# Kernel tuning notes

Measured on AMD Instinct MI355X. Metric: run time of the kernel, lower is better.

Reference implementation:

```python
import jax, jax.numpy as jnp
import numpy as np

NI = 627   # num_inputs (hardcoded 627 in original forward)
NH = 1024  # num_hidden
EPS_BN = 1e-5

def get_mask(in_f, out_f, nf, mask_type=None):
    in_deg = np.arange(in_f) % nf
    out_deg = np.arange(out_f) % nf
    if mask_type == 'output':
        out_deg = out_deg - 1
    return jnp.asarray((out_deg[:, None] >= in_deg[None, :]).astype(np.float32))

M_IN = get_mask(NI, NH, NI, 'input')        # [NH, NI]
M_H = get_mask(NH, NH, NI)                  # [NH, NH]
M_OUT = get_mask(NH, 2 * NI, NI, 'output')  # [2*NI, NH]

def masked_linear(x, W, b, mask):
    return x @ (W * mask).T + b

def conv1x1(x, W, b):
    # x: [B,C,L], W: [O,C] (kernel_size=1 conv == pointwise channel mix)
    return jnp.einsum('bcl,oc->bol', x, W) + b[None, :, None]

def bn_train(x, g, b):
    # BatchNorm1d training-mode: biased batch stats over (N, L)
    m = x.mean(axis=(0, 2), keepdims=True)
    v = x.var(axis=(0, 2), keepdims=True)
    return (x - m) * jax.lax.rsqrt(v + EPS_BN) * g[None, :, None] + b[None, :, None]

def setup_inputs() -> dict:
    key = jax.random.key(0)
    ks = iter(jax.random.split(key, 32))
    B = 512
    inputs = jax.random.randint(next(ks), (B, NI), 0, 300).astype(jnp.float32)
    def lin(k, o, i):
        return jax.random.normal(k, (o, i), jnp.float32) / np.sqrt(i)
    d = {'inputs': inputs}
    d['W_in'] = lin(next(ks), NH, NI); d['b_in'] = jnp.zeros((NH,), jnp.float32)
    d['W_h1'] = lin(next(ks), NH, NH); d['b_h1'] = jnp.zeros((NH,), jnp.float32)
    d['W_h2'] = lin(next(ks), NH, NH); d['b_h2'] = jnp.zeros((NH,), jnp.float32)
    d['W_out'] = lin(next(ks), 2 * NI, NH); d['b_out'] = jnp.zeros((2 * NI,), jnp.float32)
    chans = [(90, 1), (180, 90), (180, 180), (180, 180), (300, 180)]
    for idx, (o, c) in enumerate(chans, 1):
        d[f'cw{idx}'] = lin(next(ks), o, c)
        d[f'cb{idx}'] = jnp.zeros((o,), jnp.float32)
        if idx < 5:
            d[f'g{idx}'] = jnp.ones((o,), jnp.float32)
            d[f'be{idx}'] = jnp.zeros((o,), jnp.float32)
    return d

def reference(inputs, W_in, b_in, W_h1, b_h1, W_h2, b_h2, W_out, b_out,
              cw1, cb1, g1, be1, cw2, cb2, g2, be2, cw3, cb3, g3, be3,
              cw4, cb4, g4, be4, cw5, cb5):
    # MADE joiner + trunk (trunk = [act, ML, act, ML, ML_out])
    h = masked_linear(inputs, W_in, b_in, M_IN)
    h = jax.nn.relu(h)
    h = masked_linear(h, W_h1, b_h1, M_H)
    h = jax.nn.relu(h)
    h = masked_linear(h, W_h2, b_h2, M_H)
    out = masked_linear(h, W_out, b_out, M_OUT)      # [B, 2*NI]
    gamma_raw, theta = jnp.split(out, 2, axis=1)
    gamma = jax.nn.sigmoid(gamma_raw[:, 2:])          # [B, NI-2]
    # 1x1-conv / BN / ReLU trunk over theta viewed as [B,1,NI]
    x = theta[:, None, :]
    x = jax.nn.relu(bn_train(conv1x1(x, cw1, cb1), g1, be1))
    x = jax.nn.relu(bn_train(conv1x1(x, cw2, cb2), g2, be2))
    x = jax.nn.relu(bn_train(conv1x1(x, cw3, cb3), g3, be3))
    x = jax.nn.relu(bn_train(conv1x1(x, cw4, cb4), g4, be4))
    pred = conv1x1(x, cw5, cb5)                       # [B, 300, NI]
    logp = jax.nn.log_softmax(pred, axis=1)
    tgt = inputs.astype(jnp.int32)                    # [B, NI] class ids
    nll = -jnp.take_along_axis(logp, tgt[:, None, :], axis=1)[:, 0, :]  # [B, NI]
    ll = jnp.where(inputs[:, 2:] > 0,
                   0.1 * jnp.log(gamma + 1e-10) - nll[:, 2:],
                   0.1 * jnp.log(1.0 - gamma + 1e-10)).sum(axis=-1, keepdims=True)
    # mean cross-entropy over first two pixels (scalar, default reduction='mean')
    ll = ll - nll[:, :2].mean()
    return ll
```

## Files before the change

kernel.cpp:

```cpp
#include <hip/hip_runtime.h>
#include <hip/hip_bf16.h>
#include <math.h>

#define BATCH 512
#define NI 627
#define NH 1024
#define NOUTF 1254
#define LLEN 627
#define NBL (512 * 627)
#define EPSBN 1e-5f
#define NSLOT 10240
#define NRED2 40
#define NRED34 20

typedef __attribute__((ext_vector_type(8))) short bf16x8;
typedef __attribute__((ext_vector_type(4))) float f32x4;
typedef unsigned int uint32;
typedef unsigned short ushort16;

__device__ inline short f2b(float x) {
  __hip_bfloat16 h = __float2bfloat16(x);
  return *reinterpret_cast<short*>(&h);
}
__device__ inline float b2f(short s) {
  return __uint_as_float(((uint32)(ushort16)s) << 16);
}
__device__ inline f32x4 mfma16(bf16x8 a, bf16x8 b, f32x4 c) {
  return __builtin_amdgcn_mfma_f32_16x16x32_bf16(a, b, c, 0, 0, 0);
}
__device__ inline bf16x8 zero8() {
  bf16x8 z;
#pragma unroll
  for (int i = 0; i < 8; ++i) z[i] = 0;
  return z;
}
__device__ inline bf16x8 buildx1r(float4 alo, float4 ahi, float4 blo, float4 bhi, float th) {
  bf16x8 r;
  r[0] = f2b(fmaxf(fmaf(alo.x, th, blo.x), 0.f));
  r[1] = f2b(fmaxf(fmaf(alo.y, th, blo.y), 0.f));
  r[2] = f2b(fmaxf(fmaf(alo.z, th, blo.z), 0.f));
  r[3] = f2b(fmaxf(fmaf(alo.w, th, blo.w), 0.f));
  r[4] = f2b(fmaxf(fmaf(ahi.x, th, bhi.x), 0.f));
  r[5] = f2b(fmaxf(fmaf(ahi.y, th, bhi.y), 0.f));
  r[6] = f2b(fmaxf(fmaf(ahi.z, th, bhi.z), 0.f));
  r[7] = f2b(fmaxf(fmaf(ahi.w, th, bhi.w), 0.f));
  return r;
}
__device__ inline bf16x8 buildx1(const float* __restrict__ A1v, const float* __restrict__ B1v,
                                 int k0, float th) {
  float4 alo = *reinterpret_cast<const float4*>(&A1v[k0]);
  float4 ahi = *reinterpret_cast<const float4*>(&A1v[k0 + 4]);
  float4 blo = *reinterpret_cast<const float4*>(&B1v[k0]);
  float4 bhi = *reinterpret_cast<const float4*>(&B1v[k0 + 4]);
  return buildx1r(alo, ahi, blo, bhi, th);
}

__device__ inline void prep_mlpw_elem(const float* W, short* Wb, int i,
                                      int Nreal, int Kreal, int Kpad, int mode) {
  int n = i / Kpad, k = i - n * Kpad;
  float w = 0.f;
  if (n < Nreal && k < Kreal) {
    int od = n >= 627 ? n - 627 : n;
    int kd = k >= 627 ? k - 627 : k;
    bool keep = (mode == 0) ? (od >= k) : (mode == 1) ? (od >= kd) : (od > kd);
    if (keep) w = W[n * Kreal + k];
  }
  Wb[i] = f2b(w);
}
__device__ inline void prep_convw_elem(const float* W, short* Wb, int i,
                                       int Oreal, int Kreal, int Kpad) {
  int o = i / Kpad, k = i - o * Kpad;
  Wb[i] = (o < Oreal && k < Kreal) ? f2b(W[o * Kreal + k]) : (short)0;
}

#define PB_INB   1280
#define PB_WB1   (PB_INB + 2560)
#define PB_WB2   (PB_WB1 + 4096)
#define PB_WB3   (PB_WB2 + 4096)
#define PB_WB4   (PB_WB3 + 5120)
#define PB_CW2   (PB_WB4 + 72)
#define PB_CW3   (PB_CW2 + 144)
#define PB_CW4   (PB_CW3 + 144)
#define PB_CW5   (PB_CW4 + 240)
#define PB_CB    (PB_CW5 + 2)

__global__ __launch_bounds__(256) void prep_all(
    const float* __restrict__ inputs, short* __restrict__ INB,
    const float* __restrict__ W_in, short* __restrict__ WB1,
    const float* __restrict__ W_h1, short* __restrict__ WB2,
    const float* __restrict__ W_h2, short* __restrict__ WB3,
    const float* __restrict__ W_out, short* __restrict__ WB4,
    const float* __restrict__ cw2, short* __restrict__ CW2B,
    const float* __restrict__ cw3, short* __restrict__ CW3B,
    const float* __restrict__ cw4, short* __restrict__ CW4B,
    const float* __restrict__ cw5, short* __restrict__ CW5B,
    const float* __restrict__ cb2, const float* __restrict__ cb3,
    const float* __restrict__ cb4, const float* __restrict__ cb5,
    float* __restrict__ cb2p, float* __restrict__ cb3p,
    float* __restrict__ cb4p, float* __restrict__ cb5p)
{
  const int bid = blockIdx.x;
  if (bid < PB_INB) {
    int i = bid * 256 + threadIdx.x;
    if (i < 512 * 640) {
      int m = i / 640, k = i - m * 640;
      INB[i] = (k < NI) ? f2b(inputs[m * NI + k]) : (short)0;
    }
  } else if (bid < PB_WB1) {
    int i = (bid - PB_INB) * 256 + threadIdx.x;
    if (i < 1024 * 640) prep_mlpw_elem(W_in, WB1, i, 1024, 627, 640, 0);
  } else if (bid < PB_WB2) {
    int i = (bid - PB_WB1) * 256 + threadIdx.x;
    prep_mlpw_elem(W_h1, WB2, i, 1024, 1024, 1024, 1);
  } else if (bid < PB_WB3) {
    int i = (bid - PB_WB2) * 256 + threadIdx.x;
    prep_mlpw_elem(W_h2, WB3, i, 1024, 1024, 1024, 1);
  } else if (bid < PB_WB4) {
    int i = (bid - PB_WB3) * 256 + threadIdx.x;
    if (i < 1280 * 1024) prep_mlpw_elem(W_out, WB4, i, 1254, 1024, 1024, 2);
  } else if (bid < PB_CW2) {
    int i = (bid - PB_WB4) * 256 + threadIdx.x;
    if (i < 192 * 96) prep_convw_elem(cw2, CW2B, i, 180, 90, 96);
  } else if (bid < PB_CW3) {
    int i = (bid - PB_CW2) * 256 + threadIdx.x;
    if (i < 192 * 192) prep_convw_elem(cw3, CW3B, i, 180, 180, 192);
  } else if (bid < PB_CW4) {
    int i = (bid - PB_CW3) * 256 + threadIdx.x;
    if (i < 192 * 192) prep_convw_elem(cw4, CW4B, i, 180, 180, 192);
  } else if (bid < PB_CW5) {
    int i = (bid - PB_CW4) * 256 + threadIdx.x;
    if (i < 320 * 192) prep_convw_elem(cw5, CW5B, i, 300, 180, 192);
  } else {
    int c = (bid - PB_CW5) * 256 + threadIdx.x;
    if (c < 192) {
      cb2p[c] = (c < 180) ? cb2[c] : 0.f;
      cb3p[c] = (c < 180) ? cb3[c] : 0.f;
      cb4p[c] = (c < 180) ? cb4[c] : 0.f;
    }
    if (c < 320) cb5p[c] = (c < 300) ? cb5[c] : 0.f;
  }
}

template<int KPAD>
__global__ __launch_bounds__(256) void mlp_mfma(
    const short* __restrict__ A, const short* __restrict__ Wb, const float* __restrict__ bias,
    float* __restrict__ Cf, short* __restrict__ Cb, int Nreal, int relu)
{
  __shared__ float red[2][2][2][4][64];
  const int tid = threadIdx.x;
  const int l = tid & 63, wv = tid >> 6;
  const int wn = wv >> 1, kh = wv & 1;
  const int m0 = blockIdx.y * 32;
  const int n0 = blockIdx.x * 64 + wn * 32;
  const int lr = l & 15, lk = (l >> 4) * 8, lm4 = (l >> 4) * 4;
  f32x4 acc[2][2] = {};
  constexpr int khalf = KPAD >> 1;
  constexpr int nk = khalf >> 5;
#pragma unroll
  for (int ks = 0; ks < nk; ++ks) {
    int k0 = kh * khalf + ks * 32 + lk;
    bf16x8 a0 = *reinterpret_cast<const bf16x8*>(&A[(size_t)(m0 + lr) * KPAD + k0]);
    bf16x8 a1 = *reinterpret_cast<const bf16x8*>(&A[(size_t)(m0 + 16 + lr) * KPAD + k0]);
    bf16x8 b0 = *reinterpret_cast<const bf16x8*>(&Wb[(size_t)(n0 + lr) * KPAD + k0]);
    bf16x8 b1 = *reinterpret_cast<const bf16x8*>(&Wb[(size_t)(n0 + 16 + lr) * KPAD + k0]);
    acc[0][0] = mfma16(a0, b0, acc[0][0]);
    acc[0][1] = mfma16(a0, b1, acc[0][1]);
    acc[1][0] = mfma16(a1, b0, acc[1][0]);
    acc[1][1] = mfma16(a1, b1, acc[1][1]);
  }
  if (kh == 1) {
#pragma unroll
    for (int mi = 0; mi < 2; ++mi)
#pragma unroll
      for (int nj = 0; nj < 2; ++nj)
#pragma unroll
        for (int r = 0; r < 4; ++r) red[wn][mi][nj][r][l] = acc[mi][nj][r];
  }
  __syncthreads();
  if (kh == 0) {
#pragma unroll
    for (int mi = 0; mi < 2; ++mi)
#pragma unroll
      for (int nj = 0; nj < 2; ++nj) {
        int n = n0 + nj * 16 + lr;
        if (n >= Nreal) continue;
        float bi = bias[n];
#pragma unroll
        for (int r = 0; r < 4; ++r) {
          int m = m0 + mi * 16 + lm4 + r;
          float v = acc[mi][nj][r] + red[wn][mi][nj][r][l] + bi;
          if (relu) v = fmaxf(v, 0.f);
          if (Cb) Cb[(size_t)m * Nreal + n] = f2b(v);
          else Cf[(size_t)m * Nreal + n] = v;
        }
      }
  }
}

__global__ __launch_bounds__(256) void theta_stats(const float* __restrict__ outb, float* __restrict__ tstat)
{
  int b = blockIdx.x;
  const float* th = outb + (size_t)b * NOUTF + NI;
  float s = 0.f, q = 0.f;
  for (int l = threadIdx.x; l < LLEN; l += 256) { float t = th[l]; s += t; q += t * t; }
  for (int off = 1; off < 64; off <<= 1) { s += __shfl_xor(s, off); q += __shfl_xor(q, off); }
  __shared__ float tmp[8];
  int w = threadIdx.x >> 6;
  if ((threadIdx.x & 63) == 0) { tmp[w] = s; tmp[4 + w] = q; }
  __syncthreads();
  if (threadIdx.x == 0) {
    atomicAdd(&tstat[0], tmp[0] + tmp[1] + tmp[2] + tmp[3]);
    atomicAdd(&tstat[1], tmp[4] + tmp[5] + tmp[6] + tmp[7]);
  }
}

__global__ void finalize_conv1(const float* __restrict__ tstat, const float* __restrict__ cw1,
                               const float* __restrict__ g1, const float* __restrict__ be1,
                               float* __restrict__ a1, float* __restrict__ b1)
{
  int c = threadIdx.x;
  if (c >= 96) return;
  if (c < 90) {
    float mt = tstat[0] / (float)NBL;
    float vt = tstat[1] / (float)NBL - mt * mt;
    float w = cw1[c];
    float rs = rsqrtf(w * w * vt + EPSBN);
    float a = w * g1[c] * rs;
    a1[c] = a;
    b1[c] = be1[c] - a * mt;
  } else { a1[c] = 0.f; b1[c] = 0.f; }
}

__global__ __launch_bounds__(192) void bn_reduce1(const float* __restrict__ Sp, const float* __restrict__ Qp,
                                                  float* __restrict__ Sred, float* __restrict__ Qred)
{
  int c = threadIdx.x;
  if (c >= 180) return;
  int base = blockIdx.x * 256;
  float s = 0.f, q = 0.f;
  for (int r = 0; r < 256; ++r) {
    s += Sp[(size_t)(base + r) * 180 + c];
    q += Qp[(size_t)(base + r) * 180 + c];
  }
  Sred[blockIdx.x * 180 + c] = s;
  Qred[blockIdx.x * 180 + c] = q;
}

__global__ void finalize_bn2(const float* __restrict__ Sred, const float* __restrict__ Qred,
                             const float* __restrict__ g, const float* __restrict__ be,
                             float* __restrict__ aP, float* __restrict__ bP, int nred)
{
  int c = threadIdx.x;
  if (c >= 192) return;
  if (c < 180) {
    float s = 0.f, q = 0.f;
    for (int p = 0; p < nred; ++p) { s += Sred[p * 180 + c]; q += Qred[p * 180 + c]; }
    float m = s / (float)NBL;
    float v = q / (float)NBL - m * m;
    float a = g[c] * rsqrtf(v + EPSBN);
    aP[c] = a;
    bP[c] = be[c] - m * a;
  } else { aP[c] = 0.f; bP[c] = 0.f; }
}

__global__ __launch_bounds__(512) void conv2_stats(
    const float* __restrict__ OUTB, const float* __restrict__ A1v, const float* __restrict__ B1v,
    const short* __restrict__ cw2b, const float* __restrict__ cb2p,
    float* __restrict__ Sp, float* __restrict__ Qp)
{
  const int tid = threadIdx.x;
  const int b = blockIdx.y, j0 = blockIdx.x * 128;
  const int l = tid & 63, wv = tid >> 6, wm = wv >> 2, wn = wv & 3;
  const int lr = l & 15, lk = (l >> 4) * 8, lm4 = (l >> 4) * 4;
  const int jj0 = j0 + wn * 32 + lr, jj1 = jj0 + 16;
  const float th0 = (jj0 < LLEN) ? OUTB[(size_t)b * NOUTF + NI + jj0] : 0.f;
  const float th1 = (jj1 < LLEN) ? OUTB[(size_t)b * NOUTF + NI + jj1] : 0.f;
  f32x4 acc[6][2] = {};
#pragma unroll
  for (int ks = 0; ks < 3; ++ks) {
    int k0 = ks * 32 + lk;
    bf16x8 b0 = buildx1(A1v, B1v, k0, th0);
    bf16x8 b1 = buildx1(A1v, B1v, k0, th1);
#pragma unroll
    for (int mi = 0; mi < 6; ++mi) {
      bf16x8 av = *reinterpret_cast<const bf16x8*>(&cw2b[(wm * 96 + mi * 16 + lr) * 96 + k0]);
      acc[mi][0] = mfma16(av, b0, acc[mi][0]);
      acc[mi][1] = mfma16(av, b1, acc[mi][1]);
    }
  }
  const size_t slot = (size_t)(blockIdx.y * gridDim.x + blockIdx.x) * 4 + wn;
#pragma unroll
  for (int mi = 0; mi < 6; ++mi) {
    int m0c = wm * 96 + mi * 16 + lm4;
    float s4[4] = {0.f, 0.f, 0.f, 0.f}, q4[4] = {0.f, 0.f, 0.f, 0.f};
#pragma unroll
    for (int nj = 0; nj < 2; ++nj) {
      int jj = j0 + wn * 32 + nj * 16 + lr;
      if (jj < LLEN) {
#pragma unroll
        for (int r = 0; r < 4; ++r) {
          float v = acc[mi][nj][r] + cb2p[m0c + r];
          s4[r] += v; q4[r] += v * v;
        }
      }
    }
#pragma unroll
    for (int off = 1; off < 16; off <<= 1)
#pragma unroll
      for (int r = 0; r < 4; ++r) { s4[r] += __shfl_xor(s4[r], off); q4[r] += __shfl_xor(q4[r], off); }
    if (lr == 0) {
#pragma unroll
      for (int r = 0; r < 4; ++r) {
        int o = m0c + r;
        if (o < 180) {
          Sp[slot * 180 + o] = s4[r];
          Qp[slot * 180 + o] = q4[r];
        }
      }
    }
  }
}

__global__ __launch_bounds__(512) void fused_conv23(
    const float* __restrict__ OUTB, const float* __restrict__ A1v, const float* __restrict__ B1v,
    const short* __restrict__ cw2b, const float* __restrict__ cb2p,
    const float* __restrict__ a2, const float* __restrict__ b2,
    const short* __restrict__ cw3b, const float* __restrict__ cb3p,
    short* __restrict__ Y, float* __restrict__ Sp, float* __restrict__ Qp)
{
  __shared__ short wl2[192][98];
  __shared__ short wl3[192][196];
  __shared__ short xT2[128][196];
  const int tid = threadIdx.x;
  const int b = blockIdx.x;
  for (int t = tid; t < 192 * 12; t += 512) {
    int row = t / 12, c8 = (t - row * 12) * 8;
    *reinterpret_cast<bf16x8*>(&wl2[row][c8]) = *reinterpret_cast<const bf16x8*>(&cw2b[row * 96 + c8]);
  }
  for (int t = tid; t < 192 * 24; t += 512) {
    int row = t / 24, c8 = (t - row * 24) * 8;
    *reinterpret_cast<bf16x8*>(&wl3[row][c8]) = *reinterpret_cast<const bf16x8*>(&cw3b[row * 192 + c8]);
  }
  const int l = tid & 63, wv = tid >> 6, wm = wv >> 1, wn = wv & 1;
  const int lr = l & 15, lk = (l >> 4) * 8, lm4 = (l >> 4) * 4;
  float a2r[3][4], f2r[3][4], cb3r[3][4];
#pragma unroll
  for (int mi = 0; mi < 3; ++mi)
#pragma unroll
    for (int r = 0; r < 4; ++r) {
      int c = wm * 48 + mi * 16 + lm4 + r;
      float a = a2[c];
      a2r[mi][r] = a;
      f2r[mi][r] = fmaf(a, cb2p[c], b2[c]);
      cb3r[mi][r] = cb3p[c];
    }
  __syncthreads();
  for (int tile = 0; tile < 5; ++tile) {
    const int j0 = tile * 128;
    float th[4];
#pragma unroll
    for (int nj = 0; nj < 4; ++nj) {
      int jj = j0 + wn * 64 + nj * 16 + lr;
      th[nj] = (jj < LLEN) ? OUTB[(size_t)b * NOUTF + NI + jj] : 0.f;
    }
    f32x4 acc[3][4] = {};
#pragma unroll
    for (int ks = 0; ks < 3; ++ks) {
      int k0 = ks * 32 + lk;
      float4 alo = *reinterpret_cast<const float4*>(&A1v[k0]);
      float4 ahi = *reinterpret_cast<const float4*>(&A1v[k0 + 4]);
      float4 blo = *reinterpret_cast<const float4*>(&B1v[k0]);
      float4 bhi = *reinterpret_cast<const float4*>(&B1v[k0 + 4]);
      bf16x8 bb[4];
#pragma unroll
      for (int nj = 0; nj < 4; ++nj) bb[nj] = buildx1r(alo, ahi, blo, bhi, th[nj]);
      bf16x8 av[3];
#pragma unroll
      for (int mi = 0; mi < 3; ++mi)
        av[mi] = *reinterpret_cast<const bf16x8*>(&wl2[wm * 48 + mi * 16 + lr][k0]);
#pragma unroll
      for (int mi = 0; mi < 3; ++mi)
#pragma unroll
        for (int nj = 0; nj < 4; ++nj)
          acc[mi][nj] = mfma16(av[mi], bb[nj], acc[mi][nj]);
    }
    __syncthreads();
#pragma unroll
    for (int mi = 0; mi < 3; ++mi) {
      int m0c = wm * 48 + mi * 16 + lm4;
#pragma unroll
      for (int nj = 0; nj < 4; ++nj) {
        int col = wn * 64 + nj * 16 + lr;
        float x0 = fmaxf(fmaf(a2r[mi][0], acc[mi][nj][0], f2r[mi][0]), 0.f);
        float x1 = fmaxf(fmaf(a2r[mi][1], acc[mi][nj][1], f2r[mi][1]), 0.f);
        float x2 = fmaxf(fmaf(a2r[mi][2], acc[mi][nj][2], f2r[mi][2]), 0.f);
        float x3 = fmaxf(fmaf(a2r[mi][3], acc[mi][nj][3], f2r[mi][3]), 0.f);
        uint2 w2;
        w2.x = (uint32)(ushort16)f2b(x0) | ((uint32)(ushort16)f2b(x1) << 16);
        w2.y = (uint32)(ushort16)f2b(x2) | ((uint32)(ushort16)f2b(x3) << 16);
        *reinterpret_cast<uint2*>(&xT2[col][m0c]) = w2;
      }
    }
    __syncthreads();
    f32x4 acc2[3][4] = {};
#pragma unroll
    for (int ks = 0; ks < 6; ++ks) {
      int k0 = ks * 32 + lk;
      bf16x8 bb[4];
#pragma unroll
      for (int nj = 0; nj < 4; ++nj)
        bb[nj] = *reinterpret_cast<const bf16x8*>(&xT2[wn * 64 + nj * 16 + lr][k0]);
      bf16x8 av[3];
#pragma unroll
      for (int mi = 0; mi < 3; ++mi)
        av[mi] = *reinterpret_cast<const bf16x8*>(&wl3[wm * 48 + mi * 16 + lr][k0]);
#pragma unroll
      for (int mi = 0; mi < 3; ++mi)
#pragma unroll
        for (int nj = 0; nj < 4; ++nj)
          acc2[mi][nj] = mfma16(av[mi], bb[nj], acc2[mi][nj]);
    }
    __syncthreads();
    const size_t slot = ((size_t)b * 5 + tile) * 2 + wn;
#pragma unroll
    for (int mi = 0; mi < 3; ++mi) {
      int m0c = wm * 48 + mi * 16 + lm4;
      float s4[4] = {0.f, 0.f, 0.f, 0.f}, q4[4] = {0.f, 0.f, 0.f, 0.f};
#pragma unroll
      for (int nj = 0; nj < 4; ++nj) {
        int col = wn * 64 + nj * 16 + lr;
        int jj = j0 + col;
        float v0 = acc2[mi][nj][0] + cb3r[mi][0];
        float v1 = acc2[mi][nj][1] + cb3r[mi][1];
        float v2 = acc2[mi][nj][2] + cb3r[mi][2];
        float v3 = acc2[mi][nj][3] + cb3r[mi][3];
        if (jj < LLEN) {
          s4[0] += v0; q4[0] += v0 * v0;
          s4[1] += v1; q4[1] += v1 * v1;
          s4[2] += v2; q4[2] += v2 * v2;
          s4[3] += v3; q4[3] += v3 * v3;
        }
        uint2 w2;
        w2.x = (uint32)(ushort16)f2b(v0) | ((uint32)(ushort16)f2b(v1) << 16);
        w2.y = (uint32)(ushort16)f2b(v2) | ((uint32)(ushort16)f2b(v3) << 16);
        *reinterpret_cast<uint2*>(&xT2[col][m0c]) = w2;
      }
#pragma unroll
      for (int off = 1; off < 16; off <<= 1)
#pragma unroll
        for (int r = 0; r < 4; ++r) { s4[r] += __shfl_xor(s4[r], off); q4[r] += __shfl_xor(q4[r], off); }
      if (lr == 0) {
#pragma unroll
        for (int r = 0; r < 4; ++r) {
          int o = m0c + r;
          if (o < 180) {
            Sp[slot * 180 + o] = s4[r];
            Qp[slot * 180 + o] = q4[r];
          }
        }
      }
    }
    __syncthreads();
    for (int f = tid; f < 128 * 24; f += 512) {
      int row = f / 24, c0 = (f - row * 24) * 8;
      int jj = j0 + row;
      if (jj < LLEN) {
        bf16x8 v = *reinterpret_cast<const bf16x8*>(&xT2[row][c0]);
        *reinterpret_cast<bf16x8*>(&Y[((size_t)b * 627 + jj) * 192 + c0]) = v;
      }
    }
  }
}

__global__ __launch_bounds__(512) void conv4_ip(
    short* __restrict__ Y, const float* __restrict__ a3, const float* __restrict__ b3,
    const short* __restrict__ cw4b, const float* __restrict__ cb4p,
    float* __restrict__ Sp, float* __restrict__ Qp)
{
  __shared__ short wl4[192][196];
  __shared__ short xT[128][196];
  const int tid = threadIdx.x;
  const int b = blockIdx.x;
  for (int t = tid; t < 192 * 24; t += 512) {
    int row = t / 24, c8 = (t - row * 24) * 8;
    *reinterpret_cast<bf16x8*>(&wl4[row][c8]) = *reinterpret_cast<const bf16x8*>(&cw4b[row * 192 + c8]);
  }
  const int l = tid & 63, wv = tid >> 6, wm = wv >> 1, wn = wv & 1;
  const int lr = l & 15, lk = (l >> 4) * 8, lm4 = (l >> 4) * 4;
  float cb4r[3][4];
#pragma unroll
  for (int mi = 0; mi < 3; ++mi)
#pragma unroll
    for (int r = 0; r < 4; ++r)
      cb4r[mi][r] = cb4p[wm * 48 + mi * 16 + lm4 + r];
  for (int tile = 0; tile < 5; ++tile) {
    const int j0 = tile * 128;
    __syncthreads();
    for (int t = tid; t < 128 * 24; t += 512) {
      int col = t / 24, oct = t - col * 24;
      int jj = j0 + col;
      int c0 = oct * 8;
      bf16x8 pk;
      if (jj < LLEN) {
        bf16x8 raw = *reinterpret_cast<const bf16x8*>(&Y[((size_t)b * 627 + jj) * 192 + c0]);
        float4 alo = *reinterpret_cast<const float4*>(&a3[c0]);
        float4 ahi = *reinterpret_cast<const float4*>(&a3[c0 + 4]);
        float4 blo = *reinterpret_cast<const float4*>(&b3[c0]);
        float4 bhi = *reinterpret_cast<const float4*>(&b3[c0 + 4]);
        pk[0] = f2b(fmaxf(fmaf(alo.x, b2f(raw[0]), blo.x), 0.f));
        pk[1] = f2b(fmaxf(fmaf(alo.y, b2f(raw[1]), blo.y), 0.f));
        pk[2] = f2b(fmaxf(fmaf(alo.z, b2f(raw[2]), blo.z), 0.f));
        pk[3] = f2b(fmaxf(fmaf(alo.w, b2f(raw[3]), blo.w), 0.f));
        pk[4] = f2b(fmaxf(fmaf(ahi.x, b2f(raw[4]), bhi.x), 0.f));
        pk[5] = f2b(fmaxf(fmaf(ahi.y, b2f(raw[5]), bhi.y), 0.f));
        pk[6] = f2b(fmaxf(fmaf(ahi.z, b2f(raw[6]), bhi.z), 0.f));
        pk[7] = f2b(fmaxf(fmaf(ahi.w, b2f(raw[7]), bhi.w), 0.f));
      } else {
        pk = zero8();
      }
      *reinterpret_cast<bf16x8*>(&xT[col][c0]) = pk;
    }
    __syncthreads();
    f32x4 acc[3][4] = {};
#pragma unroll
    for (int ks = 0; ks < 6; ++ks) {
      int k0 = ks * 32 + lk;
      bf16x8 bb[4];
#pragma unroll
      for (int nj = 0; nj < 4; ++nj)
        bb[nj] = *reinterpret_cast<const bf16x8*>(&xT[wn * 64 + nj * 16 + lr][k0]);
      bf16x8 av[3];
#pragma unroll
      for (int mi = 0; mi < 3; ++mi)
        av[mi] = *reinterpret_cast<const bf16x8*>(&wl4[wm * 48 + mi * 16 + lr][k0]);
#pragma unroll
      for (int mi = 0; mi < 3; ++mi)
#pragma unroll
        for (int nj = 0; nj < 4; ++nj)
          acc[mi][nj] = mfma16(av[mi], bb[nj], acc[mi][nj]);
    }
    __syncthreads();
    const size_t slot = ((size_t)b * 5 + tile) * 2 + wn;
#pragma unroll
    for (int mi = 0; mi < 3; ++mi) {
      int m0c = wm * 48 + mi * 16 + lm4;
      float s4[4] = {0.f, 0.f, 0.f, 0.f}, q4[4] = {0.f, 0.f, 0.f, 0.f};
#pragma unroll
      for (int nj = 0; nj < 4; ++nj) {
        int col = wn * 64 + nj * 16 + lr;
        int jj = j0 + col;
        float v0 = acc[mi][nj][0] + cb4r[mi][0];
        float v1 = acc[mi][nj][1] + cb4r[mi][1];
        float v2 = acc[mi][nj][2] + cb4r[mi][2];
        float v3 = acc[mi][nj][3] + cb4r[mi][3];
        if (jj < LLEN) {
          s4[0] += v0; q4[0] += v0 * v0;
          s4[1] += v1; q4[1] += v1 * v1;
          s4[2] += v2; q4[2] += v2 * v2;
          s4[3] += v3; q4[3] += v3 * v3;
        }
        uint2 w2;
        w2.x = (uint32)(ushort16)f2b(v0) | ((uint32)(ushort16)f2b(v1) << 16);
        w2.y = (uint32)(ushort16)f2b(v2) | ((uint32)(ushort16)f2b(v3) << 16);
        *reinterpret_cast<uint2*>(&xT[col][m0c]) = w2;
      }
#pragma unroll
      for (int off = 1; off < 16; off <<= 1)
#pragma unroll
        for (int r = 0; r < 4; ++r) { s4[r] += __shfl_xor(s4[r], off); q4[r] += __shfl_xor(q4[r], off); }
      if (lr == 0) {
#pragma unroll
        for (int r = 0; r < 4; ++r) {
          int o = m0c + r;
          if (o < 180) {
            Sp[slot * 180 + o] = s4[r];
            Qp[slot * 180 + o] = q4[r];
          }
        }
      }
    }
    __syncthreads();
    for (int f = tid; f < 128 * 24; f += 512) {
      int row = f / 24, c0 = (f - row * 24) * 8;
      int jj = j0 + row;
      if (jj < LLEN) {
        bf16x8 v = *reinterpret_cast<const bf16x8*>(&xT[row][c0]);
        *reinterpret_cast<bf16x8*>(&Y[((size_t)b * 627 + jj) * 192 + c0]) = v;
      }
    }
  }
}

__global__ __launch_bounds__(512) void conv5_nll_ll(
    const short* __restrict__ Y, const float* __restrict__ a4, const float* __restrict__ b4,
    const short* __restrict__ cw5b, const float* __restrict__ cb5p,
    const float* __restrict__ inputs, const float* __restrict__ outb,
    float* __restrict__ llp, float* __restrict__ sc)
{
  __shared__ short wlds[320][200];
  __shared__ short xT[64][200];
  __shared__ int tga[640];
  __shared__ float wmax[4][64];
  __shared__ float wsum[4][64];
  __shared__ float ptgt[64];
  __shared__ float nlls[640];
  const int tid = threadIdx.x;
  const int b = blockIdx.x;
  for (int t = tid; t < 320 * 24; t += 512) {
    int row = t / 24, c8 = (t - row * 24) * 8;
    *reinterpret_cast<bf16x8*>(&wlds[row][c8]) =
        *reinterpret_cast<const bf16x8*>(&cw5b[row * 192 + c8]);
  }
  for (int t = tid; t < 640; t += 512)
    tga[t] = (t < LLEN) ? (int)inputs[(size_t)b * NI + t] : 0;
  const int l = tid & 63, wv = tid >> 6;
  const int wm = wv >> 1, wn = wv & 1;
  const int lr = l & 15, lk = (l >> 4) * 8, lm4 = (l >> 4) * 4;
  const int mf0 = wm * 5;
  float aa[3][8], bb4[3][8];
#pragma unroll
  for (int s = 0; s < 3; ++s) {
    int t = tid + s * 512;
    int c8 = (t % 24) * 8;
#pragma unroll
    for (int i = 0; i < 8; ++i) { aa[s][i] = a4[c8 + i]; bb4[s][i] = b4[c8 + i]; }
  }
  float cbr[5][4];
#pragma unroll
  for (int mi = 0; mi < 5; ++mi)
#pragma unroll
    for (int r = 0; r < 4; ++r)
      cbr[mi][r] = cb5p[(mf0 + mi) * 16 + lm4 + r];
  bf16x8 raw[3];
#pragma unroll
  for (int s = 0; s < 3; ++s) {
    int t = tid + s * 512;
    int col = t / 24, c8 = (t - col * 24) * 8;
    raw[s] = (col < LLEN) ? *reinterpret_cast<const bf16x8*>(&Y[((size_t)b * 627 + col) * 192 + c8]) : zero8();
  }
  __syncthreads();
  for (int tile = 0; tile < 10; ++tile) {
    const int l0 = tile * 64;
#pragma unroll
    for (int s = 0; s < 3; ++s) {
      int t = tid + s * 512;
      int col = t / 24, c8 = (t - col * 24) * 8;
      bf16x8 pk;
#pragma unroll
      for (int i = 0; i < 8; ++i)
        pk[i] = f2b(fmaxf(fmaf(aa[s][i], b2f(raw[s][i]), bb4[s][i]), 0.f));
      *reinterpret_cast<bf16x8*>(&xT[col][c8]) = pk;
    }
    __syncthreads();
    f32x4 acc[5][2] = {};
#pragma unroll
    for (int ks = 0; ks < 6; ++ks) {
      int k0 = ks * 32 + lk;
      bf16x8 bb0 = *reinterpret_cast<const bf16x8*>(&xT[wn * 32 + lr][k0]);
      bf16x8 bb1 = *reinterpret_cast<const bf16x8*>(&xT[wn * 32 + 16 + lr][k0]);
#pragma unroll
      for (int mi = 0; mi < 5; ++mi) {
        bf16x8 av = *reinterpret_cast<const bf16x8*>(&wlds[(mf0 + mi) * 16 + lr][k0]);
        acc[mi][0] = mfma16(av, bb0, acc[mi][0]);
        acc[mi][1] = mfma16(av, bb1, acc[mi][1]);
      }
    }
    if (tile < 9) {
#pragma unroll
      for (int s = 0; s < 3; ++s) {
        int t = tid + s * 512;
        int col = t / 24, c8 = (t - col * 24) * 8;
        int jj = l0 + 64 + col;
        raw[s] = (jj < LLEN) ? *reinterpret_cast<const bf16x8*>(&Y[((size_t)b * 627 + jj) * 192 + c8]) : zero8();
      }
    }
    float vmax0 = -1e30f, vmax1 = -1e30f;
    int t0 = tga[l0 + wn * 32 + lr], t1 = tga[l0 + wn * 32 + 16 + lr];
#pragma unroll
    for (int mi = 0; mi < 5; ++mi) {
#pragma unroll
      for (int r = 0; r < 4; ++r) {
        int m = (mf0 + mi) * 16 + lm4 + r;
        bool ok = (m < 300);
        float v0 = ok ? (acc[mi][0][r] + cbr[mi][r]) : -1e30f;
        float v1 = ok ? (acc[mi][1][r] + cbr[mi][r]) : -1e30f;
        acc[mi][0][r] = v0;
        acc[mi][1][r] = v1;
        vmax0 = fmaxf(vmax0, v0);
        vmax1 = fmaxf(vmax1, v1);
        if (m == t0) ptgt[wn * 32 + lr] = v0;
        if (m == t1) ptgt[wn * 32 + 16 + lr] = v1;
      }
    }
    vmax0 = fmaxf(vmax0, __shfl_xor(vmax0, 16)); vmax0 = fmaxf(vmax0, __shfl_xor(vmax0, 32));
    vmax1 = fmaxf(vmax1, __shfl_xor(vmax1, 16)); vmax1 = fmaxf(vmax1, __shfl_xor(vmax1, 32));
    float vs0 = 0.f, vs1 = 0.f;
#pragma unroll
    for (int mi = 0; mi < 5; ++mi)
#pragma unroll
      for (int r = 0; r < 4; ++r) {
        vs0 += __expf(acc[mi][0][r] - vmax0);
        vs1 += __expf(acc[mi][1][r] - vmax1);
      }
    vs0 += __shfl_xor(vs0, 16); vs0 += __shfl_xor(vs0, 32);
    vs1 += __shfl_xor(vs1, 16); vs1 += __shfl_xor(vs1, 32);
    if (l < 16) {
      wmax[wm][wn * 32 + lr] = vmax0; wmax[wm][wn * 32 + 16 + lr] = vmax1;
      wsum[wm][wn * 32 + lr] = vs0;   wsum[wm][wn * 32 + 16 + lr] = vs1;
    }
    __syncthreads();
    if (tid < 64) {
      int jj = l0 + tid;
      if (jj < LLEN) {
        float m0 = wmax[0][tid], m1 = wmax[1][tid], m2 = wmax[2][tid], m3 = wmax[3][tid];
        float gm = fmaxf(fmaxf(m0, m1), fmaxf(m2, m3));
        float gs = wsum[0][tid] * __expf(m0 - gm) + wsum[1][tid] * __expf(m1 - gm)
                 + wsum[2][tid] * __expf(m2 - gm) + wsum[3][tid] * __expf(m3 - gm);
        nlls[jj] = gm + logf(gs) - ptgt[tid];
      }
    }
  }
  __syncthreads();
  float s = 0.f;
  for (int lidx = 2 + tid; lidx < LLEN; lidx += 512) {
    float graw = outb[(size_t)b * NOUTF + lidx];
    float sg = 1.f / (1.f + expf(-graw));
    float term = (tga[lidx] > 0) ? (0.1f * logf(sg + 1e-10f) - nlls[lidx])
                                 : (0.1f * logf(1.f - sg + 1e-10f));
    s += term;
  }
  for (int off = 1; off < 64; off <<= 1) s += __shfl_xor(s, off);
  if (l == 0) wmax[0][wv] = s;
  __syncthreads();
  if (tid == 0) {
    float tot = 0.f;
#pragma unroll
    for (int w = 0; w < 8; ++w) tot += wmax[0][w];
    llp[b] = tot;
    atomicAdd(sc, nlls[0] + nlls[1]);
  }
}

__global__ void ll_pass2(const float* __restrict__ llp, const float* __restrict__ sc, float* __restrict__ outp)
{
  int i = blockIdx.x * blockDim.x + threadIdx.x;
  if (i < BATCH) outp[i] = llp[i] - sc[0] * (1.f / 1024.f);
}

extern "C" void kernel_launch(void* const* d_in, const int* in_sizes, int n_in,
                              void* d_out, int out_size, void* d_ws, size_t ws_size,
                              hipStream_t stream)
{
  const float* inputs = (const float*)d_in[0];
  const float* W_in = (const float*)d_in[1];
  const float* b_in = (const float*)d_in[2];
  const float* W_h1 = (const float*)d_in[3];
  const float* b_h1 = (const float*)d_in[4];
  const float* W_h2 = (const float*)d_in[5];
  const float* b_h2 = (const float*)d_in[6];
  const float* W_out = (const float*)d_in[7];
  const float* b_out = (const float*)d_in[8];
  const float* cw1 = (const float*)d_in[9];
  const float* g1 = (const float*)d_in[11];
  const float* be1 = (const float*)d_in[12];
  const float* cw2 = (const float*)d_in[13];
  const float* cb2 = (const float*)d_in[14];
  const float* g2 = (const float*)d_in[15];
  const float* be2 = (const float*)d_in[16];
  const float* cw3 = (const float*)d_in[17];
  const float* cb3 = (const float*)d_in[18];
  const float* g3 = (const float*)d_in[19];
  const float* be3 = (const float*)d_in[20];
  const float* cw4 = (const float*)d_in[21];
  const float* cb4 = (const float*)d_in[22];
  const float* g4 = (const float*)d_in[23];
  const float* be4 = (const float*)d_in[24];
  const float* cw5 = (const float*)d_in[25];
  const float* cb5 = (const float*)d_in[26];

  char* p = (char*)d_ws;
  short* Y = (short*)p;    p += (size_t)512 * 627 * 192 * 2;
  short* INB = (short*)p;  p += (size_t)512 * 640 * 2;
  short* HB1 = (short*)p;  p += (size_t)512 * 1024 * 2;
  short* HB2 = (short*)p;  p += (size_t)512 * 1024 * 2;
  short* HB3 = (short*)p;  p += (size_t)512 * 1024 * 2;
  short* WB1 = (short*)p;  p += (size_t)1024 * 640 * 2;
  short* WB2 = (short*)p;  p += (size_t)1024 * 1024 * 2;
  short* WB3 = (short*)p;  p += (size_t)1024 * 1024 * 2;
  short* WB4 = (short*)p;  p += (size_t)1280 * 1024 * 2;
  short* CW2B = (short*)p; p += (size_t)192 * 96 * 2;
  short* CW3B = (short*)p; p += (size_t)192 * 192 * 2;
  short* CW4B = (short*)p; p += (size_t)192 * 192 * 2;
  short* CW5B = (short*)p; p += (size_t)320 * 192 * 2;
  float* fp = (float*)p;
  float* OUTB = fp;  fp += (size_t)512 * 1254;
  float* NLLB = fp;  fp += 321028;
  float* LLP = fp;   fp += 512;
  float* A1 = fp;    fp += 96;
  float* B1g = fp;   fp += 96;
  float* A2 = fp;    fp += 192;
  float* B2g = fp;   fp += 192;
  float* A3 = fp;    fp += 192;
  float* B3g = fp;   fp += 192;
  float* A4 = fp;    fp += 192;
  float* B4g = fp;   fp += 192;
  float* CB2P = fp;  fp += 192;
  float* CB3P = fp;  fp += 192;
  float* CB4P = fp;  fp += 192;
  float* CB5P = fp;  fp += 320;
  float* TST = fp;   fp += 2;
  float* SC = fp;    fp += 2;
  float* SPP = fp;   fp += (size_t)NSLOT * 180;
  float* QPP = fp;   fp += (size_t)NSLOT * 180;
  float* SRED = fp;  fp += NRED2 * 180;
  float* QRED = fp;  fp += NRED2 * 180;
  (void)NLLB;

  hipMemsetAsync(TST, 0, 4 * sizeof(float), stream);

  prep_all<<<dim3(PB_CB), 256, 0, stream>>>(
      inputs, INB, W_in, WB1, W_h1, WB2, W_h2, WB3, W_out, WB4,
      cw2, CW2B, cw3, CW3B, cw4, CW4B, cw5, CW5B,
      cb2, cb3, cb4, cb5, CB2P, CB3P, CB4P, CB5P);

  mlp_mfma<640><<<dim3(16, 16), 256, 0, stream>>>(INB, WB1, b_in, nullptr, HB1, 1024, 1);
  mlp_mfma<1024><<<dim3(16, 16), 256, 0, stream>>>(HB1, WB2, b_h1, nullptr, HB2, 1024, 1);
  mlp_mfma<1024><<<dim3(16, 16), 256, 0, stream>>>(HB2, WB3, b_h2, nullptr, HB3, 1024, 0);
  mlp_mfma<1024><<<dim3(20, 16), 256, 0, stream>>>(HB3, WB4, b_out, OUTB, nullptr, 1254, 0);

  theta_stats<<<dim3(BATCH), 256, 0, stream>>>(OUTB, TST);
  finalize_conv1<<<1, 96, 0, stream>>>(TST, cw1, g1, be1, A1, B1g);

  conv2_stats<<<dim3(5, BATCH), 512, 0, stream>>>(OUTB, A1, B1g, CW2B, CB2P, SPP, QPP);
  bn_reduce1<<<dim3(NRED2), 192, 0, stream>>>(SPP, QPP, SRED, QRED);
  finalize_bn2<<<1, 192, 0, stream>>>(SRED, QRED, g2, be2, A2, B2g, NRED2);

  fused_conv23<<<dim3(BATCH), 512, 0, stream>>>(OUTB, A1, B1g, CW2B, CB2P, A2, B2g, CW3B, CB3P, Y, SPP, QPP);
  bn_reduce1<<<dim3(NRED34), 192, 0, stream>>>(SPP, QPP, SRED, QRED);
  finalize_bn2<<<1, 192, 0, stream>>>(SRED, QRED, g3, be3, A3, B3g, NRED34);

  conv4_ip<<<dim3(BATCH), 512, 0, stream>>>(Y, A3, B3g, CW4B, CB4P, SPP, QPP);
  bn_reduce1<<<dim3(NRED34), 192, 0, stream>>>(SPP, QPP, SRED, QRED);
  finalize_bn2<<<1, 192, 0, stream>>>(SRED, QRED, g4, be4, A4, B4g, NRED34);

  conv5_nll_ll<<<dim3(BATCH), 512, 0, stream>>>(Y, A4, B4g, CW5B, CB5P, inputs, OUTB, LLP, SC);

  ll_pass2<<<dim3(2), 256, 0, stream>>>(LLP, SC, (float*)d_out);
}
```

Before: 505.1 us.

## Split conv4 into per-tile blocks with register-resident weights

Conv4 is relaunched as a 2D grid of (10 tiles × batch) blocks of 256 threads, each handling 64 positions, instead of one 512-thread block per batch row looping over five 128-wide tiles. The weight matrix is loaded directly into registers per wave rather than staged into shared memory, which shrinks LDS use and should raise occupancy and parallelism. The trade-off is that every block reloads its weight slice from global memory and register pressure goes up. Partial-stat slot indexing changes to b*10+tile, which is consistent with the previous slot count of 10 per batch.

```diff
diff --git a/kernel.cpp b/kernel.cpp
--- a/kernel.cpp
+++ b/kernel.cpp
@@ -472,121 +472,116 @@
   }
 }
 
-__global__ __launch_bounds__(512) void conv4_ip(
+__global__ __launch_bounds__(256) void conv4_rw(
     short* __restrict__ Y, const float* __restrict__ a3, const float* __restrict__ b3,
     const short* __restrict__ cw4b, const float* __restrict__ cb4p,
     float* __restrict__ Sp, float* __restrict__ Qp)
 {
-  __shared__ short wl4[192][196];
-  __shared__ short xT[128][196];
+  __shared__ short xT[64][196];
   const int tid = threadIdx.x;
-  const int b = blockIdx.x;
-  for (int t = tid; t < 192 * 24; t += 512) {
-    int row = t / 24, c8 = (t - row * 24) * 8;
-    *reinterpret_cast<bf16x8*>(&wl4[row][c8]) = *reinterpret_cast<const bf16x8*>(&cw4b[row * 192 + c8]);
-  }
-  const int l = tid & 63, wv = tid >> 6, wm = wv >> 1, wn = wv & 1;
+  const int b = blockIdx.y, tile = blockIdx.x, j0 = tile * 64;
+  const int l = tid & 63, wm = tid >> 6;
   const int lr = l & 15, lk = (l >> 4) * 8, lm4 = (l >> 4) * 4;
+  bf16x8 wreg[3][6];
+#pragma unroll
+  for (int mi = 0; mi < 3; ++mi)
+#pragma unroll
+    for (int ks = 0; ks < 6; ++ks)
+      wreg[mi][ks] = *reinterpret_cast<const bf16x8*>(&cw4b[(wm * 48 + mi * 16 + lr) * 192 + ks * 32 + lk]);
   float cb4r[3][4];
 #pragma unroll
   for (int mi = 0; mi < 3; ++mi)
 #pragma unroll
     for (int r = 0; r < 4; ++r)
       cb4r[mi][r] = cb4p[wm * 48 + mi * 16 + lm4 + r];
-  for (int tile = 0; tile < 5; ++tile) {
-    const int j0 = tile * 128;
-    __syncthreads();
-    for (int t = tid; t < 128 * 24; t += 512) {
-      int col = t / 24, oct = t - col * 24;
+  for (int t = tid; t < 64 * 24; t += 256) {
+    int col = t / 24, oct = t - col * 24;
+    int jj = j0 + col;
+    int c0 = oct * 8;
+    bf16x8 pk;
+    if (jj < LLEN) {
+      bf16x8 raw = *reinterpret_cast<const bf16x8*>(&Y[((size_t)b * 627 + jj) * 192 + c0]);
+      float4 alo = *reinterpret_cast<const float4*>(&a3[c0]);
+      float4 ahi = *reinterpret_cast<const float4*>(&a3[c0 + 4]);
+      float4 blo = *reinterpret_cast<const float4*>(&b3[c0]);
+      float4 bhi = *reinterpret_cast<const float4*>(&b3[c0 + 4]);
+      pk[0] = f2b(fmaxf(fmaf(alo.x, b2f(raw[0]), blo.x), 0.f));
+      pk[1] = f2b(fmaxf(fmaf(alo.y, b2f(raw[1]), blo.y), 0.f));
+      pk[2] = f2b(fmaxf(fmaf(alo.z, b2f(raw[2]), blo.z), 0.f));
+      pk[3] = f2b(fmaxf(fmaf(alo.w, b2f(raw[3]), blo.w), 0.f));
+      pk[4] = f2b(fmaxf(fmaf(ahi.x, b2f(raw[4]), bhi.x), 0.f));
+      pk[5] = f2b(fmaxf(fmaf(ahi.y, b2f(raw[5]), bhi.y), 0.f));
+      pk[6] = f2b(fmaxf(fmaf(ahi.z, b2f(raw[6]), bhi.z), 0.f));
+      pk[7] = f2b(fmaxf(fmaf(ahi.w, b2f(raw[7]), bhi.w), 0.f));
+    } else {
+      pk = zero8();
+    }
+    *reinterpret_cast<bf16x8*>(&xT[col][c0]) = pk;
+  }
+  __syncthreads();
+  f32x4 acc[3][4] = {};
+#pragma unroll
+  for (int ks = 0; ks < 6; ++ks) {
+    int k0 = ks * 32 + lk;
+    bf16x8 bb0 = *reinterpret_cast<const bf16x8*>(&xT[lr][k0]);
+    bf16x8 bb1 = *reinterpret_cast<const bf16x8*>(&xT[16 + lr][k0]);
+    bf16x8 bb2 = *reinterpret_cast<const bf16x8*>(&xT[32 + lr][k0]);
+    bf16x8 bb3 = *reinterpret_cast<const bf16x8*>(&xT[48 + lr][k0]);
+#pragma unroll
+    for (int mi = 0; mi < 3; ++mi) {
+      acc[mi][0] = mfma16(wreg[mi][ks], bb0, acc[mi][0]);
+      acc[mi][1] = mfma16(wreg[mi][ks], bb1, acc[mi][1]);
+      acc[mi][2] = mfma16(wreg[mi][ks], bb2, acc[mi][2]);
+      acc[mi][3] = mfma16(wreg[mi][ks], bb3, acc[mi][3]);
+    }
+  }
+  __syncthreads();
+  const size_t slot = (size_t)b * 10 + tile;
+#pragma unroll
+  for (int mi = 0; mi < 3; ++mi) {
+    int m0c = wm * 48 + mi * 16 + lm4;
+    float s4[4] = {0.f, 0.f, 0.f, 0.f}, q4[4] = {0.f, 0.f, 0.f, 0.f};
+#pragma unroll
+    for (int nj = 0; nj < 4; ++nj) {
+      int col = nj * 16 + lr;
       int jj = j0 + col;
-      int c0 = oct * 8;
-      bf16x8 pk;
+      float v0 = acc[mi][nj][0] + cb4r[mi][0];
+      float v1 = acc[mi][nj][1] + cb4r[mi][1];
+      float v2 = acc[mi][nj][2] + cb4r[mi][2];
+      float v3 = acc[mi][nj][3] + cb4r[mi][3];
       if (jj < LLEN) {
-        bf16x8 raw = *reinterpret_cast<const bf16x8*>(&Y[((size_t)b * 627 + jj) * 192 + c0]);
-        float4 alo = *reinterpret_cast<const float4*>(&a3[c0]);
-        float4 ahi = *reinterpret_cast<const float4*>(&a3[c0 + 4]);
-        float4 blo = *reinterpret_cast<const float4*>(&b3[c0]);
-        float4 bhi = *reinterpret_cast<const float4*>(&b3[c0 + 4]);
-        pk[0] = f2b(fmaxf(fmaf(alo.x, b2f(raw[0]), blo.x), 0.f));
-        pk[1] = f2b(fmaxf(fmaf(alo.y, b2f(raw[1]), blo.y), 0.f));
-        pk[2] = f2b(fmaxf(fmaf(alo.z, b2f(raw[2]), blo.z), 0.f));
-        pk[3] = f2b(fmaxf(fmaf(alo.w, b2f(raw[3]), blo.w), 0.f));
-        pk[4] = f2b(fmaxf(fmaf(ahi.x, b2f(raw[4]), bhi.x), 0.f));
-        pk[5] = f2b(fmaxf(fmaf(ahi.y, b2f(raw[5]), bhi.y), 0.f));
-        pk[6] = f2b(fmaxf(fmaf(ahi.z, b2f(raw[6]), bhi.z), 0.f));
-        pk[7] = f2b(fmaxf(fmaf(ahi.w, b2f(raw[7]), bhi.w), 0.f));
-      } else {
-        pk = zero8();
-      }
-      *reinterpret_cast<bf16x8*>(&xT[col][c0]) = pk;
-    }
-    __syncthreads();
-    f32x4 acc[3][4] = {};
-#pragma unroll
-    for (int ks = 0; ks < 6; ++ks) {
-      int k0 = ks * 32 + lk;
-      bf16x8 bb[4];
-#pragma unroll
-      for (int nj = 0; nj < 4; ++nj)
-        bb[nj] = *reinterpret_cast<const bf16x8*>(&xT[wn * 64 + nj * 16 + lr][k0]);
-      bf16x8 av[3];
-#pragma unroll
-      for (int mi = 0; mi < 3; ++mi)
-        av[mi] = *reinterpret_cast<const bf16x8*>(&wl4[wm * 48 + mi * 16 + lr][k0]);
-#pragma unroll
-      for (int mi = 0; mi < 3; ++mi)
-#pragma unroll
-        for (int nj = 0; nj < 4; ++nj)
-          acc[mi][nj] = mfma16(av[mi], bb[nj], acc[mi][nj]);
-    }
-    __syncthreads();
-    const size_t slot = ((size_t)b * 5 + tile) * 2 + wn;
-#pragma unroll
-    for (int mi = 0; mi < 3; ++mi) {
-      int m0c = wm * 48 + mi * 16 + lm4;
-      float s4[4] = {0.f, 0.f, 0.f, 0.f}, q4[4] = {0.f, 0.f, 0.f, 0.f};
-#pragma unroll
-      for (int nj = 0; nj < 4; ++nj) {
-        int col = wn * 64 + nj * 16 + lr;
-        int jj = j0 + col;
-        float v0 = acc[mi][nj][0] + cb4r[mi][0];
-        float v1 = acc[mi][nj][1] + cb4r[mi][1];
-        float v2 = acc[mi][nj][2] + cb4r[mi][2];
-        float v3 = acc[mi][nj][3] + cb4r[mi][3];
-        if (jj < LLEN) {
-          s4[0] += v0; q4[0] += v0 * v0;
-          s4[1] += v1; q4[1] += v1 * v1;
-          s4[2] += v2; q4[2] += v2 * v2;
-          s4[3] += v3; q4[3] += v3 * v3;
+        s4[0] += v0; q4[0] += v0 * v0;
+        s4[1] += v1; q4[1] += v1 * v1;
+        s4[2] += v2; q4[2] += v2 * v2;
+        s4[3] += v3; q4[3] += v3 * v3;
+      }
+      uint2 w2;
+      w2.x = (uint32)(ushort16)f2b(v0) | ((uint32)(ushort16)f2b(v1) << 16);
+      w2.y = (uint32)(ushort16)f2b(v2) | ((uint32)(ushort16)f2b(v3) << 16);
+      *reinterpret_cast<uint2*>(&xT[col][m0c]) = w2;
+    }
+#pragma unroll
+    for (int off = 1; off < 16; off <<= 1)
+#pragma unroll
+      for (int r = 0; r < 4; ++r) { s4[r] += __shfl_xor(s4[r], off); q4[r] += __shfl_xor(q4[r], off); }
+    if (lr == 0) {
+#pragma unroll
+      for (int r = 0; r < 4; ++r) {
+        int o = m0c + r;
+        if (o < 180) {
+          Sp[slot * 180 + o] = s4[r];
+          Qp[slot * 180 + o] = q4[r];
         }
-        uint2 w2;
-        w2.x = (uint32)(ushort16)f2b(v0) | ((uint32)(ushort16)f2b(v1) << 16);
-        w2.y = (uint32)(ushort16)f2b(v2) | ((uint32)(ushort16)f2b(v3) << 16);
-        *reinterpret_cast<uint2*>(&xT[col][m0c]) = w2;
-      }
-#pragma unroll
-      for (int off = 1; off < 16; off <<= 1)
-#pragma unroll
-        for (int r = 0; r < 4; ++r) { s4[r] += __shfl_xor(s4[r], off); q4[r] += __shfl_xor(q4[r], off); }
-      if (lr == 0) {
-#pragma unroll
-        for (int r = 0; r < 4; ++r) {
-          int o = m0c + r;
-          if (o < 180) {
-            Sp[slot * 180 + o] = s4[r];
-            Qp[slot * 180 + o] = q4[r];
-          }
-        }
-      }
-    }
-    __syncthreads();
-    for (int f = tid; f < 128 * 24; f += 512) {
-      int row = f / 24, c0 = (f - row * 24) * 8;
-      int jj = j0 + row;
-      if (jj < LLEN) {
-        bf16x8 v = *reinterpret_cast<const bf16x8*>(&xT[row][c0]);
-        *reinterpret_cast<bf16x8*>(&Y[((size_t)b * 627 + jj) * 192 + c0]) = v;
-      }
+      }
+    }
+  }
+  __syncthreads();
+  for (int f = tid; f < 64 * 24; f += 256) {
+    int row = f / 24, c0 = (f - row * 24) * 8;
+    int jj = j0 + row;
+    if (jj < LLEN) {
+      bf16x8 v = *reinterpret_cast<const bf16x8*>(&xT[row][c0]);
+      *reinterpret_cast<bf16x8*>(&Y[((size_t)b * 627 + jj) * 192 + c0]) = v;
     }
   }
 }
@@ -839,7 +834,7 @@
   bn_reduce1<<<dim3(NRED34), 192, 0, stream>>>(SPP, QPP, SRED, QRED);
   finalize_bn2<<<1, 192, 0, stream>>>(SRED, QRED, g3, be3, A3, B3g, NRED34);
 
-  conv4_ip<<<dim3(BATCH), 512, 0, stream>>>(Y, A3, B3g, CW4B, CB4P, SPP, QPP);
+  conv4_rw<<<dim3(10, BATCH), 256, 0, stream>>>(Y, A3, B3g, CW4B, CB4P, SPP, QPP);
   bn_reduce1<<<dim3(NRED34), 192, 0, stream>>>(SPP, QPP, SRED, QRED);
   finalize_bn2<<<1, 192, 0, stream>>>(SRED, QRED, g4, be4, A4, B4g, NRED34);
 
```

New measurement: 528.0 us. +4.5%, slower.

## Prefetch next conv4 tile into registers and accumulate BN stats across tiles

Applied to the files above, without the earlier changes.

In conv4_ip, the global load of the next 128-column tile of Y now goes into registers while the current tile's MFMA runs, so memory latency overlaps compute. The BN scale and shift vectors are staged once in shared memory. Per-tile partial sums are kept in registers and reduced once per block, which cuts the partial-stat slots and shrinks the following bn_reduce1 grid. The cost is 6 extra bf16x8 registers per thread and an extra barrier per tile; the reduce grid size must match the new slot count.

```diff
diff --git a/kernel.cpp b/kernel.cpp
--- a/kernel.cpp
+++ b/kernel.cpp
@@ -12,6 +12,7 @@
 #define NSLOT 10240
 #define NRED2 40
 #define NRED34 20
+#define NRED4 4
 
 typedef __attribute__((ext_vector_type(8))) short bf16x8;
 typedef __attribute__((ext_vector_type(4))) float f32x4;
@@ -479,12 +480,14 @@
 {
   __shared__ short wl4[192][196];
   __shared__ short xT[128][196];
+  __shared__ float ab[384];
   const int tid = threadIdx.x;
   const int b = blockIdx.x;
   for (int t = tid; t < 192 * 24; t += 512) {
     int row = t / 24, c8 = (t - row * 24) * 8;
     *reinterpret_cast<bf16x8*>(&wl4[row][c8]) = *reinterpret_cast<const bf16x8*>(&cw4b[row * 192 + c8]);
   }
+  for (int t = tid; t < 384; t += 512) ab[t] = (t < 192) ? a3[t] : b3[t - 192];
   const int l = tid & 63, wv = tid >> 6, wm = wv >> 1, wn = wv & 1;
   const int lr = l & 15, lk = (l >> 4) * 8, lm4 = (l >> 4) * 4;
   float cb4r[3][4];
@@ -493,32 +496,31 @@
 #pragma unroll
     for (int r = 0; r < 4; ++r)
       cb4r[mi][r] = cb4p[wm * 48 + mi * 16 + lm4 + r];
+  bf16x8 raw[6];
+#pragma unroll
+  for (int s = 0; s < 6; ++s) {
+    int t = tid + s * 512;
+    int col = t / 24, c8 = (t - col * 24) * 8;
+    raw[s] = (col < LLEN) ? *reinterpret_cast<const bf16x8*>(&Y[((size_t)b * 627 + col) * 192 + c8]) : zero8();
+  }
+  float sacc[3][4] = {}, qacc[3][4] = {};
+  __syncthreads();
   for (int tile = 0; tile < 5; ++tile) {
     const int j0 = tile * 128;
-    __syncthreads();
-    for (int t = tid; t < 128 * 24; t += 512) {
-      int col = t / 24, oct = t - col * 24;
+#pragma unroll
+    for (int s = 0; s < 6; ++s) {
+      int t = tid + s * 512;
+      int col = t / 24, c8 = (t - col * 24) * 8;
       int jj = j0 + col;
-      int c0 = oct * 8;
       bf16x8 pk;
       if (jj < LLEN) {
-        bf16x8 raw = *reinterpret_cast<const bf16x8*>(&Y[((size_t)b * 627 + jj) * 192 + c0]);
-        float4 alo = *reinterpret_cast<const float4*>(&a3[c0]);
-        float4 ahi = *reinterpret_cast<const float4*>(&a3[c0 + 4]);
-        float4 blo = *reinterpret_cast<const float4*>(&b3[c0]);
-        float4 bhi = *reinterpret_cast<const float4*>(&b3[c0 + 4]);
-        pk[0] = f2b(fmaxf(fmaf(alo.x, b2f(raw[0]), blo.x), 0.f));
-        pk[1] = f2b(fmaxf(fmaf(alo.y, b2f(raw[1]), blo.y), 0.f));
-        pk[2] = f2b(fmaxf(fmaf(alo.z, b2f(raw[2]), blo.z), 0.f));
-        pk[3] = f2b(fmaxf(fmaf(alo.w, b2f(raw[3]), blo.w), 0.f));
-        pk[4] = f2b(fmaxf(fmaf(ahi.x, b2f(raw[4]), bhi.x), 0.f));
-        pk[5] = f2b(fmaxf(fmaf(ahi.y, b2f(raw[5]), bhi.y), 0.f));
-        pk[6] = f2b(fmaxf(fmaf(ahi.z, b2f(raw[6]), bhi.z), 0.f));
-        pk[7] = f2b(fmaxf(fmaf(ahi.w, b2f(raw[7]), bhi.w), 0.f));
+#pragma unroll
+        for (int i = 0; i < 8; ++i)
+          pk[i] = f2b(fmaxf(fmaf(ab[c8 + i], b2f(raw[s][i]), ab[192 + c8 + i]), 0.f));
       } else {
         pk = zero8();
       }
-      *reinterpret_cast<bf16x8*>(&xT[col][c0]) = pk;
+      *reinterpret_cast<bf16x8*>(&xT[col][c8]) = pk;
     }
     __syncthreads();
     f32x4 acc[3][4] = {};
@@ -539,12 +541,19 @@
         for (int nj = 0; nj < 4; ++nj)
           acc[mi][nj] = mfma16(av[mi], bb[nj], acc[mi][nj]);
     }
-    __syncthreads();
-    const size_t slot = ((size_t)b * 5 + tile) * 2 + wn;
+    if (tile < 4) {
+#pragma unroll
+      for (int s = 0; s < 6; ++s) {
+        int t = tid + s * 512;
+        int col = t / 24, c8 = (t - col * 24) * 8;
+        int jj = j0 + 128 + col;
+        raw[s] = (jj < LLEN) ? *reinterpret_cast<const bf16x8*>(&Y[((size_t)b * 627 + jj) * 192 + c8]) : zero8();
+      }
+    }
+    __syncthreads();
 #pragma unroll
     for (int mi = 0; mi < 3; ++mi) {
       int m0c = wm * 48 + mi * 16 + lm4;
-      float s4[4] = {0.f, 0.f, 0.f, 0.f}, q4[4] = {0.f, 0.f, 0.f, 0.f};
 #pragma unroll
       for (int nj = 0; nj < 4; ++nj) {
         int col = wn * 64 + nj * 16 + lr;
@@ -554,29 +563,15 @@
         float v2 = acc[mi][nj][2] + cb4r[mi][2];
         float v3 = acc[mi][nj][3] + cb4r[mi][3];
         if (jj < LLEN) {
-          s4[0] += v0; q4[0] += v0 * v0;
-          s4[1] += v1; q4[1] += v1 * v1;
-          s4[2] += v2; q4[2] += v2 * v2;
-          s4[3] += v3; q4[3] += v3 * v3;
+          sacc[mi][0] += v0; qacc[mi][0] += v0 * v0;
+          sacc[mi][1] += v1; qacc[mi][1] += v1 * v1;
+          sacc[mi][2] += v2; qacc[mi][2] += v2 * v2;
+          sacc[mi][3] += v3; qacc[mi][3] += v3 * v3;
         }
         uint2 w2;
         w2.x = (uint32)(ushort16)f2b(v0) | ((uint32)(ushort16)f2b(v1) << 16);
         w2.y = (uint32)(ushort16)f2b(v2) | ((uint32)(ushort16)f2b(v3) << 16);
         *reinterpret_cast<uint2*>(&xT[col][m0c]) = w2;
-      }
-#pragma unroll
-      for (int off = 1; off < 16; off <<= 1)
-#pragma unroll
-        for (int r = 0; r < 4; ++r) { s4[r] += __shfl_xor(s4[r], off); q4[r] += __shfl_xor(q4[r], off); }
-      if (lr == 0) {
-#pragma unroll
-        for (int r = 0; r < 4; ++r) {
-          int o = m0c + r;
-          if (o < 180) {
-            Sp[slot * 180 + o] = s4[r];
-            Qp[slot * 180 + o] = q4[r];
-          }
-        }
       }
     }
     __syncthreads();
@@ -586,6 +581,29 @@
       if (jj < LLEN) {
         bf16x8 v = *reinterpret_cast<const bf16x8*>(&xT[row][c0]);
         *reinterpret_cast<bf16x8*>(&Y[((size_t)b * 627 + jj) * 192 + c0]) = v;
+      }
+    }
+    __syncthreads();
+  }
+  const size_t slot = (size_t)b * 2 + wn;
+#pragma unroll
+  for (int mi = 0; mi < 3; ++mi) {
+#pragma unroll
+    for (int off = 1; off < 16; off <<= 1)
+#pragma unroll
+      for (int r = 0; r < 4; ++r) {
+        sacc[mi][r] += __shfl_xor(sacc[mi][r], off);
+        qacc[mi][r] += __shfl_xor(qacc[mi][r], off);
+      }
+    if (lr == 0) {
+      int m0c = wm * 48 + mi * 16 + lm4;
+#pragma unroll
+      for (int r = 0; r < 4; ++r) {
+        int o = m0c + r;
+        if (o < 180) {
+          Sp[slot * 180 + o] = sacc[mi][r];
+          Qp[slot * 180 + o] = qacc[mi][r];
+        }
       }
     }
   }
@@ -840,8 +858,8 @@
   finalize_bn2<<<1, 192, 0, stream>>>(SRED, QRED, g3, be3, A3, B3g, NRED34);
 
   conv4_ip<<<dim3(BATCH), 512, 0, stream>>>(Y, A3, B3g, CW4B, CB4P, SPP, QPP);
-  bn_reduce1<<<dim3(NRED34), 192, 0, stream>>>(SPP, QPP, SRED, QRED);
-  finalize_bn2<<<1, 192, 0, stream>>>(SRED, QRED, g4, be4, A4, B4g, NRED34);
+  bn_reduce1<<<dim3(NRED4), 192, 0, stream>>>(SPP, QPP, SRED, QRED);
+  finalize_bn2<<<1, 192, 0, stream>>>(SRED, QRED, g4, be4, A4, B4g, NRED4);
 
   conv5_nll_ll<<<dim3(BATCH), 512, 0, stream>>>(Y, A4, B4g, CW5B, CB5P, inputs, OUTB, LLP, SC);
 
```

Result: faster. 471.2 us (-6.7%).
